# Kernel tuning notes

Measured on AMD Instinct MI355X. Metric: run time of the kernel, lower is better.

The kernel has to match this reference:

```python
import jax, jax.numpy as jnp
import numpy as np

N, E, B = 16384, 65536, 32
D_IN, ED, H, L = 4, 5, 64, 3  # node feat, edge feat, hidden=output, num layers
NEG_SLOPE = 0.1
EPS = 1e-5


def _leaky(v):
    return jnp.where(v > 0, v, NEG_SLOPE * v)


def setup_inputs() -> dict:
    key = jax.random.key(0)
    ks = jax.random.split(key, 32)
    s = 0.05
    inp = {
        'x': jax.random.normal(ks[0], (N, D_IN), jnp.float32),
        'edge_index': jax.random.randint(ks[1], (2, E), 0, N),
        'edge_attr': jax.random.normal(ks[2], (E, ED), jnp.float32),
        'batch': jnp.sort(jax.random.randint(ks[3], (N,), 0, B)),
        # input projection Linear(4 -> H)
        'W_in': s * jax.random.normal(ks[4], (H, D_IN), jnp.float32),
        'b_in': jnp.zeros((H,), jnp.float32),
        # per-layer edge MLP: Linear(ED->H), Linear(H->H), Linear(H->H*H); stacked over L
        'ew1': s * jax.random.normal(ks[5], (L, H, ED), jnp.float32),
        'eb1': jnp.zeros((L, H), jnp.float32),
        'ew2': s * jax.random.normal(ks[6], (L, H, H), jnp.float32),
        'eb2': jnp.zeros((L, H), jnp.float32),
        'ew3': s * jax.random.normal(ks[7], (L, H * H, H), jnp.float32),
        'eb3': jnp.zeros((L, H * H), jnp.float32),
        # NNConv root weight + bias per layer
        'root_w': s * jax.random.normal(ks[8], (L, H, H), jnp.float32),
        'root_b': jnp.zeros((L, H), jnp.float32),
        # LayerNorm per layer
        'ln_g': jnp.ones((L, H), jnp.float32),
        'ln_b': jnp.zeros((L, H), jnp.float32),
        # prediction head: Linear(H->H), Linear(H->H//2), Linear(H//2->1)
        'pw1': s * jax.random.normal(ks[9], (H, H), jnp.float32),
        'pb1': jnp.zeros((H,), jnp.float32),
        'pw2': s * jax.random.normal(ks[10], (H // 2, H), jnp.float32),
        'pb2': jnp.zeros((H // 2,), jnp.float32),
        'pw3': s * jax.random.normal(ks[11], (1, H // 2), jnp.float32),
        'pb3': jnp.zeros((1,), jnp.float32),
    }
    return inp


def reference(x, edge_index, edge_attr, batch, W_in, b_in, ew1, eb1, ew2, eb2,
              ew3, eb3, root_w, root_b, ln_g, ln_b, pw1, pb1, pw2, pb2, pw3, pb3):
    src, dst = edge_index[0], edge_index[1]
    n_nodes = x.shape[0]
    n_edges = edge_attr.shape[0]
    # in-degree for scatter-mean (PyG yields 0 for isolated nodes)
    deg = jax.ops.segment_sum(jnp.ones((n_edges,), x.dtype), dst, num_segments=n_nodes)
    deg = jnp.maximum(deg, 1.0)[:, None]

    # input projection (dropout = identity in eval)
    h = _leaky(x @ W_in.T + b_in)

    for l in range(L):
        # edge MLP -> per-edge weight matrix [E, H, H]
        e = _leaky(edge_attr @ ew1[l].T + eb1[l])
        e = _leaky(e @ ew2[l].T + eb2[l])
        Wf = (e @ ew3[l].T + eb3[l]).reshape(n_edges, H, H)
        # message = x_src @ W_edge, scatter-mean to dst
        msg = jnp.einsum('ei,eio->eo', h[src], Wf)
        agg = jax.ops.segment_sum(msg, dst, num_segments=n_nodes) / deg
        out = agg + h @ root_w[l].T + root_b[l]
        # LayerNorm (post-norm)
        mu = out.mean(-1, keepdims=True)
        var = ((out - mu) ** 2).mean(-1, keepdims=True)
        out = (out - mu) * jax.lax.rsqrt(var + EPS) * ln_g[l] + ln_b[l]
        # activation + (identity) dropout + residual (in==out for all layers)
        h = _leaky(out) + h

    # global mean pool over graphs
    pooled = jax.ops.segment_sum(h, batch, num_segments=B)
    cnt = jax.ops.segment_sum(jnp.ones((n_nodes,), h.dtype), batch, num_segments=B)
    pooled = pooled / jnp.maximum(cnt, 1.0)[:, None]

    # prediction head
    p = _leaky(pooled @ pw1.T + pb1)
    p = _leaky(p @ pw2.T + pb2)
    pred = (p @ pw3.T + pb3).squeeze(-1)  # [B]
    return pred
```

## Files before the change

kernel.cpp:

```cpp
#include <hip/hip_runtime.h>
#include <hip/hip_bf16.h>

#define N_NODES 16384
#define N_EDGES 65536
#define NB      32
#define H       64
#define NLAYERS 3
#define NEG     0.1f
#define LN_EPS  1e-5f

typedef _Float16 f16;
typedef _Float16 f16x2 __attribute__((ext_vector_type(2)));
typedef _Float16 f16x8 __attribute__((ext_vector_type(8)));
typedef __fp16   hf16x2 __attribute__((ext_vector_type(2)));
typedef float    f32x16 __attribute__((ext_vector_type(16)));

union F16x8 { f16x8 v; f16x2 p[4]; int4 i4; int2 i2[2]; };
union F16x2U { f16x2 h2; hf16x2 raw; unsigned int u; };
union F16U   { f16 h; unsigned short u; };

__device__ __forceinline__ f16x2 pkrtz(float a, float b) {
    F16x2U t; t.raw = __builtin_amdgcn_cvt_pkrtz(a, b); return t.h2;
}
__device__ __forceinline__ float leaky(float v) { return v > 0.f ? v : NEG * v; }

__global__ __launch_bounds__(256) void k_setup(const float* __restrict__ x,
                                               const float* __restrict__ Win,
                                               const float* __restrict__ bin,
                                               const int* __restrict__ dst,
                                               const float* __restrict__ ew3,
                                               const float* __restrict__ eb3,
                                               float* __restrict__ h,
                                               float* __restrict__ deg,
                                               f16* __restrict__ Bp) {
    int bid = blockIdx.x;
    if (bid < 4096) {
        int t = bid * 256 + threadIdx.x;
        int n = t >> 6, j = t & 63;
        const float* xr = x + n * 4;
        const float* wr = Win + j * 4;
        float v = bin[j] + xr[0] * wr[0] + xr[1] * wr[1] + xr[2] * wr[2] + xr[3] * wr[3];
        h[t] = leaky(v);
    } else if (bid < 4352) {
        int e = (bid - 4096) * 256 + threadIdx.x;
        atomicAdd(&deg[dst[e]], 1.0f);
    } else {
        int tg    = (bid - 4352) * 256 + threadIdx.x;
        int lane  = tg & 63;
        int gslot = tg >> 6;
        int l     = gslot / 520;
        int slot  = gslot - l * 520;
        const float* ew3l = ew3 + (size_t)l * 262144;
        const float* eb3l = eb3 + (size_t)l * 4096;
        int i   = slot >> 3;
        int rem = slot & 7;
        int ks  = rem >> 1;
        int oq  = rem & 1;
        int o   = oq * 32 + (lane & 31);
        int k0  = ks * 16 + (lane >> 5) * 8;
        float v[8];
        if (i < 64) {
            const float* s = ew3l + ((size_t)(i * 64 + o)) * 64 + k0;
            float4 a = ((const float4*)s)[0];
            float4 b = ((const float4*)s)[1];
            v[0] = a.x; v[1] = a.y; v[2] = a.z; v[3] = a.w;
            v[4] = b.x; v[5] = b.y; v[6] = b.z; v[7] = b.w;
        } else {
#pragma unroll
            for (int j = 0; j < 8; j++) v[j] = eb3l[(k0 + j) * 64 + o];
        }
        union { int4 i4; f16 a[8]; } out;
#pragma unroll
        for (int j = 0; j < 8; j++) out.a[j] = (f16)v[j];
        *(int4*)(Bp + (size_t)l * 266240 + (size_t)slot * 512 + lane * 8) = out.i4;
    }
}

#define HS_STRIDE 76

__device__ __forceinline__ void loadB8(const f16* __restrict__ Bp, int c, int oq, int lane, F16x8* dstB) {
    const f16* base = Bp + (((size_t)(c * 16 + oq)) << 9) + lane * 8;
#pragma unroll
    for (int di = 0; di < 2; di++)
#pragma unroll
        for (int ks = 0; ks < 4; ks++)
            dstB[di * 4 + ks].i4 = *(const int4*)(base + ((di * 8 + ks * 2) << 9));
}
__device__ __forceinline__ void loadB4(const f16* __restrict__ Bp, int oq, int lane, F16x8* dstB) {
    const f16* base = Bp + (((size_t)(512 + oq)) << 9) + lane * 8;
#pragma unroll
    for (int ks = 0; ks < 4; ks++)
        dstB[ks].i4 = *(const int4*)(base + ((ks * 2) << 9));
}

__device__ __forceinline__ void msg_chunk2(int c, const F16x8* __restrict__ B,
                                           const unsigned short* hp0,
                                           const unsigned short* hp1,
                                           const f16x2 (*e2p)[4][4], f32x16* CC) {
    unsigned int rr0 = *(const unsigned int*)(hp0 + 2 * c);
    unsigned int rr1 = *(const unsigned int*)(hp1 + 2 * c);
    F16x2U h00, h01, h10, h11;
    h00.u = __builtin_amdgcn_perm(rr0, rr0, 0x01000100u);
    h10.u = __builtin_amdgcn_perm(rr0, rr0, 0x03020302u);
    h01.u = __builtin_amdgcn_perm(rr1, rr1, 0x01000100u);
    h11.u = __builtin_amdgcn_perm(rr1, rr1, 0x03020302u);
#pragma unroll
    for (int ks = 0; ks < 4; ks++) {
        F16x8 A00, A01, A10, A11;
#pragma unroll
        for (int r = 0; r < 4; r++) {
            A00.p[r] = h00.h2 * e2p[0][ks][r];
            A01.p[r] = h01.h2 * e2p[1][ks][r];
            A10.p[r] = h10.h2 * e2p[0][ks][r];
            A11.p[r] = h11.h2 * e2p[1][ks][r];
        }
        CC[0] = __builtin_amdgcn_mfma_f32_32x32x16_f16(A00.v, B[0 * 4 + ks].v, CC[0], 0, 0, 0);
        CC[1] = __builtin_amdgcn_mfma_f32_32x32x16_f16(A01.v, B[0 * 4 + ks].v, CC[1], 0, 0, 0);
        CC[2] = __builtin_amdgcn_mfma_f32_32x32x16_f16(A10.v, B[1 * 4 + ks].v, CC[2], 0, 0, 0);
        CC[3] = __builtin_amdgcn_mfma_f32_32x32x16_f16(A11.v, B[1 * 4 + ks].v, CC[3], 0, 0, 0);
    }
}

__global__ __launch_bounds__(256, 2) void k_msg(const float* __restrict__ h,
                                                const float* __restrict__ ea,
                                                const float* __restrict__ w1,
                                                const float* __restrict__ b1,
                                                const float* __restrict__ w2,
                                                const float* __restrict__ b2,
                                                const f16* __restrict__ Bp,
                                                const int* __restrict__ src,
                                                const int* __restrict__ dst,
                                                float* __restrict__ agg) {
    __shared__ __align__(16) unsigned short hsL[128 * HS_STRIDE];
    __shared__ __align__(16) unsigned short e1L[128 * 72];
    __shared__ __align__(16) unsigned short e2L[128 * 72];
    __shared__ float eas[128 * 8];
    __shared__ int dstL[128];

    const int t    = threadIdx.x;
    const int lane = t & 63;
    const int w    = t >> 6;
    const int eh   = w >> 1, oq = w & 1;
    const int m    = lane & 31;
    const int kp   = lane >> 5;
    const int eb   = blockIdx.x * 128;

    for (int idx = t; idx < 640; idx += 256) {
        int r = idx / 5, d = idx - r * 5;
        eas[r * 8 + d] = ea[(size_t)eb * 5 + idx];
    }
    {
        int e    = t >> 1;
        int half = t & 1;
        int nsrc = src[eb + e];
        const float4* hr = (const float4*)(h + (size_t)nsrc * 64 + half * 32);
        unsigned int* hrow = (unsigned int*)hsL + e * (HS_STRIDE / 2) + half * 16;
#pragma unroll
        for (int q = 0; q < 8; q++) {
            float4 v = hr[q];
            F16x2U p0, p1;
            p0.raw = __builtin_amdgcn_cvt_pkrtz(v.x, v.y);
            p1.raw = __builtin_amdgcn_cvt_pkrtz(v.z, v.w);
            hrow[q * 2 + 0] = p0.u;
            hrow[q * 2 + 1] = p1.u;
        }
        if (t < 128) dstL[t] = dst[eb + t];
    }
    __syncthreads();

    {
        int kk = t & 63;
        int eg = t >> 6;
        float w1r[5];
#pragma unroll
        for (int d = 0; d < 5; d++) w1r[d] = w1[kk * 5 + d];
        float b1r = b1[kk];
#pragma unroll 4
        for (int g = 0; g < 32; g++) {
            int row = eg * 32 + g;
            float4 a4 = *(const float4*)(eas + row * 8);
            float a5 = eas[row * 8 + 4];
            float v = b1r + a4.x * w1r[0] + a4.y * w1r[1] + a4.z * w1r[2] + a4.w * w1r[3] + a5 * w1r[4];
            F16U z; z.h = (f16)leaky(v);
            e1L[row * 72 + kk] = z.u;
        }
    }
    __syncthreads();

    {
        F16x8 W2f[4];
#pragma unroll
        for (int ks = 0; ks < 4; ks++) {
            const float* s = w2 + (size_t)(oq * 32 + m) * 64 + ks * 16 + kp * 8;
            float4 a = ((const float4*)s)[0];
            float4 b = ((const float4*)s)[1];
            W2f[ks].p[0] = pkrtz(a.x, a.y);
            W2f[ks].p[1] = pkrtz(a.z, a.w);
            W2f[ks].p[2] = pkrtz(b.x, b.y);
            W2f[ks].p[3] = pkrtz(b.z, b.w);
        }
        float b2r = b2[oq * 32 + m];
#pragma unroll
        for (int tt = 0; tt < 2; tt++) {
            f32x16 C2 = {0,0,0,0,0,0,0,0,0,0,0,0,0,0,0,0};
#pragma unroll
            for (int ks = 0; ks < 4; ks++) {
                F16x8 A;
                A.i4 = *(const int4*)(e1L + (size_t)((eh * 2 + tt) * 32 + m) * 72 + ks * 16 + kp * 8);
                C2 = __builtin_amdgcn_mfma_f32_32x32x16_f16(A.v, W2f[ks].v, C2, 0, 0, 0);
            }
#pragma unroll
            for (int reg = 0; reg < 16; reg++) {
                int r = (reg & 3) + 8 * (reg >> 2) + 4 * kp;
                F16U z; z.h = (f16)leaky(C2[reg] + b2r);
                e2L[((eh * 2 + tt) * 32 + r) * 72 + oq * 32 + m] = z.u;
            }
        }
    }
    __syncthreads();

    f16x2 e2p[2][4][4];
#pragma unroll
    for (int tt = 0; tt < 2; tt++) {
#pragma unroll
        for (int ks = 0; ks < 4; ks++) {
            F16x8 q;
            q.i4 = *(const int4*)(e2L + (size_t)((eh * 2 + tt) * 32 + m) * 72 + ks * 16 + kp * 8);
            e2p[tt][ks][0] = q.p[0]; e2p[tt][ks][1] = q.p[1];
            e2p[tt][ks][2] = q.p[2]; e2p[tt][ks][3] = q.p[3];
        }
    }

    f32x16 CC[4];
#pragma unroll
    for (int q = 0; q < 4; q++)
#pragma unroll
        for (int r = 0; r < 16; r++) CC[q][r] = 0.f;

    const unsigned short* hp0 = hsL + ((eh * 2 + 0) * 32 + m) * HS_STRIDE;
    const unsigned short* hp1 = hsL + ((eh * 2 + 1) * 32 + m) * HS_STRIDE;

    F16x8 B0[8], B1[8];
    loadB8(Bp, 0, oq, lane, B0);
    loadB8(Bp, 1, oq, lane, B1);
    for (int it = 0; it < 15; it++) {
        int c = it * 2;
        msg_chunk2(c,     B0, hp0, hp1, e2p, CC);  loadB8(Bp, c + 2, oq, lane, B0);
        msg_chunk2(c + 1, B1, hp0, hp1, e2p, CC);  loadB8(Bp, c + 3, oq, lane, B1);
    }
    msg_chunk2(30, B0, hp0, hp1, e2p, CC);
    loadB4(Bp, oq, lane, B0);
    msg_chunk2(31, B1, hp0, hp1, e2p, CC);

#pragma unroll
    for (int ks = 0; ks < 4; ks++) {
        int koff = (ks * 16 + kp * 8) * 2;
        const char* r0p = (const char*)hsL + (size_t)((eh * 2 + 0) * 32 + m) * (HS_STRIDE * 2) + koff;
        const char* r1p = (const char*)hsL + (size_t)((eh * 2 + 1) * 32 + m) * (HS_STRIDE * 2) + koff;
        F16x8 A0, A1;
        A0.i2[0] = *(const int2*)(r0p); A0.i2[1] = *(const int2*)(r0p + 8);
        A1.i2[0] = *(const int2*)(r1p); A1.i2[1] = *(const int2*)(r1p + 8);
        CC[0] = __builtin_amdgcn_mfma_f32_32x32x16_f16(A0.v, B0[ks].v, CC[0], 0, 0, 0);
        CC[1] = __builtin_amdgcn_mfma_f32_32x32x16_f16(A1.v, B0[ks].v, CC[1], 0, 0, 0);
    }

    int o = oq * 32 + m;
#pragma unroll
    for (int reg = 0; reg < 16; reg++) {
        int r = (reg & 3) + 8 * (reg >> 2) + 4 * kp;
        atomicAdd(&agg[(size_t)dstL[(eh * 2 + 0) * 32 + r] * 64 + o], CC[0][reg] + CC[2][reg]);
    }
#pragma unroll
    for (int reg = 0; reg < 16; reg++) {
        int r = (reg & 3) + 8 * (reg >> 2) + 4 * kp;
        atomicAdd(&agg[(size_t)dstL[(eh * 2 + 1) * 32 + r] * 64 + o], CC[1][reg] + CC[3][reg]);
    }
}

__global__ __launch_bounds__(256) void k_node(const float* __restrict__ agg,
                                              const float* __restrict__ deg,
                                              const float* __restrict__ rw,
                                              const float* __restrict__ rb,
                                              const float* __restrict__ lg,
                                              const float* __restrict__ lb,
                                              float* __restrict__ h,
                                              const int* __restrict__ batch,
                                              float* __restrict__ pooled,
                                              int last) {
    __shared__ __align__(16) unsigned short hA[64 * 72];
    __shared__ float outL[64][68];
    int t = threadIdx.x;
    int nb = blockIdx.x * 64;
    int lane = t & 63, w = t >> 6;
    int nq = w >> 1, oq = w & 1;
    int m = lane & 31, kp = lane >> 5;

    {
        int r = t >> 2, c0 = (t & 3) * 16;
        const float4* hr = (const float4*)(h + (size_t)(nb + r) * 64 + c0);
        unsigned int* drow = (unsigned int*)hA + r * 36 + c0 / 2;
#pragma unroll
        for (int q = 0; q < 4; q++) {
            float4 v = hr[q];
            F16x2U p0, p1;
            p0.raw = __builtin_amdgcn_cvt_pkrtz(v.x, v.y);
            p1.raw = __builtin_amdgcn_cvt_pkrtz(v.z, v.w);
            drow[q * 2] = p0.u; drow[q * 2 + 1] = p1.u;
        }
    }
    F16x8 Bf[4];
#pragma unroll
    for (int ks = 0; ks < 4; ks++) {
        const float* s = rw + (size_t)(oq * 32 + m) * 64 + ks * 16 + kp * 8;
        float4 a = ((const float4*)s)[0];
        float4 b = ((const float4*)s)[1];
        Bf[ks].p[0] = pkrtz(a.x, a.y);
        Bf[ks].p[1] = pkrtz(a.z, a.w);
        Bf[ks].p[2] = pkrtz(b.x, b.y);
        Bf[ks].p[3] = pkrtz(b.z, b.w);
    }
    __syncthreads();

    f32x16 C = {0,0,0,0,0,0,0,0,0,0,0,0,0,0,0,0};
#pragma unroll
    for (int ks = 0; ks < 4; ks++) {
        F16x8 A;
        A.i4 = *(const int4*)(hA + (size_t)(nq * 32 + m) * 72 + ks * 16 + kp * 8);
        C = __builtin_amdgcn_mfma_f32_32x32x16_f16(A.v, Bf[ks].v, C, 0, 0, 0);
    }

    int o = oq * 32 + m;
#pragma unroll
    for (int reg = 0; reg < 16; reg++) {
        int r = (reg & 3) + 8 * (reg >> 2) + 4 * kp;
        int n = nq * 32 + r;
        outL[n][o] = C[reg] + rb[o] + agg[(size_t)(nb + n) * 64 + o] / fmaxf(deg[nb + n], 1.0f);
    }
    __syncthreads();

    float gj = lg[lane], bj = lb[lane];
    float accp = 0.f;
    int cur = batch[nb + w * 16];
    for (int q = 0; q < 16; q++) {
        int n = w * 16 + q;
        float v = outL[n][lane];
        float mu = v;
#pragma unroll
        for (int msk = 32; msk > 0; msk >>= 1) mu += __shfl_xor(mu, msk);
        mu *= (1.f / 64.f);
        float d = v - mu;
        float var = d * d;
#pragma unroll
        for (int msk = 32; msk > 0; msk >>= 1) var += __shfl_xor(var, msk);
        var *= (1.f / 64.f);
        float ov = d * rsqrtf(var + LN_EPS) * gj + bj;
        float hn = leaky(ov) + h[(size_t)(nb + n) * 64 + lane];
        h[(size_t)(nb + n) * 64 + lane] = hn;
        if (last) {
            int b = batch[nb + n];
            if (b != cur) { atomicAdd(&pooled[cur * 64 + lane], accp); accp = 0.f; cur = b; }
            accp += hn;
        }
    }
    if (last) atomicAdd(&pooled[cur * 64 + lane], accp);
}

__global__ __launch_bounds__(256) void k_head(const float* __restrict__ pooled,
                                              const int* __restrict__ batch,
                                              const float* __restrict__ pw1, const float* __restrict__ pb1,
                                              const float* __restrict__ pw2, const float* __restrict__ pb2,
                                              const float* __restrict__ pw3, const float* __restrict__ pb3,
                                              float* __restrict__ out) {
    __shared__ float cntL[32];
    __shared__ float ps[32][64];
    __shared__ float p1[32][64];
    __shared__ float p2[32][32];
    int t = threadIdx.x;
    if (t < 32) cntL[t] = 0.f;
    __syncthreads();
    {
        const int4* bp4 = (const int4*)(batch + t * 64);
        int cur = batch[t * 64];
        float c = 0.f;
        for (int q = 0; q < 16; q++) {
            int4 b4 = bp4[q];
            int bs[4] = { b4.x, b4.y, b4.z, b4.w };
#pragma unroll
            for (int e = 0; e < 4; e++) {
                if (bs[e] != cur) { atomicAdd(&cntL[cur], c); cur = bs[e]; c = 0.f; }
                c += 1.f;
            }
        }
        atomicAdd(&cntL[cur], c);
    }
    __syncthreads();
    for (int idx = t; idx < 2048; idx += 256) {
        int b = idx >> 6, j = idx & 63;
        ps[b][j] = pooled[idx] / fmaxf(cntL[b], 1.0f);
    }
    __syncthreads();
    for (int idx = t; idx < 2048; idx += 256) {
        int b = idx >> 6, j = idx & 63;
        float v = pb1[j];
#pragma unroll 8
        for (int i = 0; i < 64; i++) v += ps[b][i] * pw1[j * 64 + i];
        p1[b][j] = leaky(v);
    }
    __syncthreads();
    for (int idx = t; idx < 1024; idx += 256) {
        int b = idx >> 5, j = idx & 31;
        float v = pb2[j];
#pragma unroll 8
        for (int i = 0; i < 64; i++) v += p1[b][i] * pw2[j * 64 + i];
        p2[b][j] = leaky(v);
    }
    __syncthreads();
    if (t < 32) {
        float v = pb3[0];
#pragma unroll 8
        for (int i = 0; i < 32; i++) v += p2[t][i] * pw3[i];
        out[t] = v;
    }
}

extern "C" void kernel_launch(void* const* d_in, const int* in_sizes, int n_in,
                              void* d_out, int out_size, void* d_ws, size_t ws_size,
                              hipStream_t stream) {
    const float* x    = (const float*)d_in[0];
    const int*   eidx = (const int*)  d_in[1];
    const float* ea   = (const float*)d_in[2];
    const int*   bat  = (const int*)  d_in[3];
    const float* Win  = (const float*)d_in[4];
    const float* bin  = (const float*)d_in[5];
    const float* ew1  = (const float*)d_in[6];
    const float* eb1  = (const float*)d_in[7];
    const float* ew2  = (const float*)d_in[8];
    const float* eb2  = (const float*)d_in[9];
    const float* ew3  = (const float*)d_in[10];
    const float* eb3  = (const float*)d_in[11];
    const float* rw   = (const float*)d_in[12];
    const float* rb   = (const float*)d_in[13];
    const float* lg   = (const float*)d_in[14];
    const float* lb   = (const float*)d_in[15];
    const float* pw1  = (const float*)d_in[16];
    const float* pb1  = (const float*)d_in[17];
    const float* pw2  = (const float*)d_in[18];
    const float* pb2  = (const float*)d_in[19];
    const float* pw3  = (const float*)d_in[20];
    const float* pb3  = (const float*)d_in[21];
    float* out = (float*)d_out;

    float* ws     = (float*)d_ws;
    float* h      = ws;
    float* agg    = ws + 1048576;
    float* deg    = ws + 4194304;
    float* pooled = ws + 4210688;
    f16*   Bp     = (f16*)(ws + 4212800);

    const int* srcp = eidx;
    const int* dstp = eidx + N_EDGES;

    (void)hipMemsetAsync(agg, 0, (size_t)3164224 * sizeof(float), stream);

    k_setup<<<4742, 256, 0, stream>>>(x, Win, bin, dstp, ew3, eb3, h, deg, Bp);

    for (int l = 0; l < NLAYERS; l++) {
        float* agg_l = agg + (size_t)l * N_NODES * H;
        k_msg <<<N_EDGES / 128, 256, 0, stream>>>(h, ea, ew1 + l * 320, eb1 + l * 64,
                                                  ew2 + l * 4096, eb2 + l * 64,
                                                  Bp + (size_t)l * 266240,
                                                  srcp, dstp, agg_l);
        k_node<<<N_NODES / 64, 256, 0, stream>>>(agg_l, deg, rw + l * 4096, rb + l * 64,
                                                 lg + l * 64, lb + l * 64, h,
                                                 bat, pooled, l == NLAYERS - 1 ? 1 : 0);
    }

    k_head<<<1, 256, 0, stream>>>(pooled, bat, pw1, pb1, pw2, pb2, pw3, pb3, out);
}
```

Measured before the change: 323.1 us.

## Fuse all layers into one persistent cooperative kernel with grid syncs

Measured after the change: 596.5 us. 84.6% more time.

```diff
diff --git a/kernel.cpp b/kernel.cpp
--- a/kernel.cpp
+++ b/kernel.cpp
@@ -1,5 +1,8 @@
 #include <hip/hip_runtime.h>
 #include <hip/hip_bf16.h>
+#include <hip/hip_cooperative_groups.h>
+
+namespace cg = cooperative_groups;
 
 #define N_NODES 16384
 #define N_EDGES 65536
@@ -24,59 +27,26 @@
 }
 __device__ __forceinline__ float leaky(float v) { return v > 0.f ? v : NEG * v; }
 
-__global__ __launch_bounds__(256) void k_setup(const float* __restrict__ x,
-                                               const float* __restrict__ Win,
-                                               const float* __restrict__ bin,
-                                               const int* __restrict__ dst,
-                                               const float* __restrict__ ew3,
-                                               const float* __restrict__ eb3,
-                                               float* __restrict__ h,
-                                               float* __restrict__ deg,
-                                               f16* __restrict__ Bp) {
-    int bid = blockIdx.x;
-    if (bid < 4096) {
-        int t = bid * 256 + threadIdx.x;
-        int n = t >> 6, j = t & 63;
-        const float* xr = x + n * 4;
-        const float* wr = Win + j * 4;
-        float v = bin[j] + xr[0] * wr[0] + xr[1] * wr[1] + xr[2] * wr[2] + xr[3] * wr[3];
-        h[t] = leaky(v);
-    } else if (bid < 4352) {
-        int e = (bid - 4096) * 256 + threadIdx.x;
-        atomicAdd(&deg[dst[e]], 1.0f);
-    } else {
-        int tg    = (bid - 4352) * 256 + threadIdx.x;
-        int lane  = tg & 63;
-        int gslot = tg >> 6;
-        int l     = gslot / 520;
-        int slot  = gslot - l * 520;
-        const float* ew3l = ew3 + (size_t)l * 262144;
-        const float* eb3l = eb3 + (size_t)l * 4096;
-        int i   = slot >> 3;
-        int rem = slot & 7;
-        int ks  = rem >> 1;
-        int oq  = rem & 1;
-        int o   = oq * 32 + (lane & 31);
-        int k0  = ks * 16 + (lane >> 5) * 8;
-        float v[8];
-        if (i < 64) {
-            const float* s = ew3l + ((size_t)(i * 64 + o)) * 64 + k0;
-            float4 a = ((const float4*)s)[0];
-            float4 b = ((const float4*)s)[1];
-            v[0] = a.x; v[1] = a.y; v[2] = a.z; v[3] = a.w;
-            v[4] = b.x; v[5] = b.y; v[6] = b.z; v[7] = b.w;
-        } else {
-#pragma unroll
-            for (int j = 0; j < 8; j++) v[j] = eb3l[(k0 + j) * 64 + o];
-        }
-        union { int4 i4; f16 a[8]; } out;
-#pragma unroll
-        for (int j = 0; j < 8; j++) out.a[j] = (f16)v[j];
-        *(int4*)(Bp + (size_t)l * 266240 + (size_t)slot * 512 + lane * 8) = out.i4;
-    }
-}
-
 #define HS_STRIDE 76
+
+struct MsgSh {
+    unsigned short hsL[128 * HS_STRIDE];
+    unsigned short e1L[128 * 72];
+    unsigned short e2L[128 * 72];
+    float eas[128 * 8];
+    int dstL[128];
+};
+struct NodeSh {
+    unsigned short hA[64 * 72];
+    float outL[64][68];
+};
+struct HeadSh {
+    float cntL[32];
+    float ps[32][64];
+    float p1[32][64];
+    float p2[32][32];
+};
+union ShU { MsgSh m[2]; NodeSh n; HeadSh hd; };
 
 __device__ __forceinline__ void loadB8(const f16* __restrict__ Bp, int c, int oq, int lane, F16x8* dstB) {
     const f16* base = Bp + (((size_t)(c * 16 + oq)) << 9) + lane * 8;
@@ -121,40 +91,33 @@
     }
 }
 
-__global__ __launch_bounds__(256, 2) void k_msg(const float* __restrict__ h,
-                                                const float* __restrict__ ea,
-                                                const float* __restrict__ w1,
-                                                const float* __restrict__ b1,
-                                                const float* __restrict__ w2,
-                                                const float* __restrict__ b2,
-                                                const f16* __restrict__ Bp,
-                                                const int* __restrict__ src,
-                                                const int* __restrict__ dst,
-                                                float* __restrict__ agg) {
-    __shared__ __align__(16) unsigned short hsL[128 * HS_STRIDE];
-    __shared__ __align__(16) unsigned short e1L[128 * 72];
-    __shared__ __align__(16) unsigned short e2L[128 * 72];
-    __shared__ float eas[128 * 8];
-    __shared__ int dstL[128];
-
-    const int t    = threadIdx.x;
-    const int lane = t & 63;
-    const int w    = t >> 6;
-    const int eh   = w >> 1, oq = w & 1;
+__device__ void msg_phase(MsgSh& S, int th, int ebh,
+                          const float* __restrict__ h,
+                          const float* __restrict__ ea,
+                          const float* __restrict__ w1,
+                          const float* __restrict__ b1,
+                          const float* __restrict__ w2,
+                          const float* __restrict__ b2,
+                          const f16* __restrict__ Bp,
+                          const int* __restrict__ src,
+                          const int* __restrict__ dst,
+                          float* __restrict__ agg) {
+    const int lane = th & 63;
+    const int wl   = th >> 6;
+    const int eh   = wl >> 1, oq = wl & 1;
     const int m    = lane & 31;
     const int kp   = lane >> 5;
-    const int eb   = blockIdx.x * 128;
-
-    for (int idx = t; idx < 640; idx += 256) {
+
+    for (int idx = th; idx < 640; idx += 256) {
         int r = idx / 5, d = idx - r * 5;
-        eas[r * 8 + d] = ea[(size_t)eb * 5 + idx];
+        S.eas[r * 8 + d] = ea[(size_t)ebh * 5 + idx];
     }
     {
-        int e    = t >> 1;
-        int half = t & 1;
-        int nsrc = src[eb + e];
-        const float4* hr = (const float4*)(h + (size_t)nsrc * 64 + half * 32);
-        unsigned int* hrow = (unsigned int*)hsL + e * (HS_STRIDE / 2) + half * 16;
+        int e    = th >> 1;
+        int half2 = th & 1;
+        int nsrc = src[ebh + e];
+        const float4* hr = (const float4*)(h + (size_t)nsrc * 64 + half2 * 32);
+        unsigned int* hrow = (unsigned int*)S.hsL + e * (HS_STRIDE / 2) + half2 * 16;
 #pragma unroll
         for (int q = 0; q < 8; q++) {
             float4 v = hr[q];
@@ -164,13 +127,13 @@
             hrow[q * 2 + 0] = p0.u;
             hrow[q * 2 + 1] = p1.u;
         }
-        if (t < 128) dstL[t] = dst[eb + t];
+        if (th < 128) S.dstL[th] = dst[ebh + th];
     }
     __syncthreads();
 
     {
-        int kk = t & 63;
-        int eg = t >> 6;
+        int kk = th & 63;
+        int eg = th >> 6;
         float w1r[5];
 #pragma unroll
         for (int d = 0; d < 5; d++) w1r[d] = w1[kk * 5 + d];
@@ -178,11 +141,11 @@
 #pragma unroll 4
         for (int g = 0; g < 32; g++) {
             int row = eg * 32 + g;
-            float4 a4 = *(const float4*)(eas + row * 8);
-            float a5 = eas[row * 8 + 4];
+            float4 a4 = *(const float4*)(S.eas + row * 8);
+            float a5 = S.eas[row * 8 + 4];
             float v = b1r + a4.x * w1r[0] + a4.y * w1r[1] + a4.z * w1r[2] + a4.w * w1r[3] + a5 * w1r[4];
             F16U z; z.h = (f16)leaky(v);
-            e1L[row * 72 + kk] = z.u;
+            S.e1L[row * 72 + kk] = z.u;
         }
     }
     __syncthreads();
@@ -206,14 +169,14 @@
 #pragma unroll
             for (int ks = 0; ks < 4; ks++) {
                 F16x8 A;
-                A.i4 = *(const int4*)(e1L + (size_t)((eh * 2 + tt) * 32 + m) * 72 + ks * 16 + kp * 8);
+                A.i4 = *(const int4*)(S.e1L + (size_t)((eh * 2 + tt) * 32 + m) * 72 + ks * 16 + kp * 8);
                 C2 = __builtin_amdgcn_mfma_f32_32x32x16_f16(A.v, W2f[ks].v, C2, 0, 0, 0);
             }
 #pragma unroll
             for (int reg = 0; reg < 16; reg++) {
                 int r = (reg & 3) + 8 * (reg >> 2) + 4 * kp;
                 F16U z; z.h = (f16)leaky(C2[reg] + b2r);
-                e2L[((eh * 2 + tt) * 32 + r) * 72 + oq * 32 + m] = z.u;
+                S.e2L[((eh * 2 + tt) * 32 + r) * 72 + oq * 32 + m] = z.u;
             }
         }
     }
@@ -225,7 +188,7 @@
 #pragma unroll
         for (int ks = 0; ks < 4; ks++) {
             F16x8 q;
-            q.i4 = *(const int4*)(e2L + (size_t)((eh * 2 + tt) * 32 + m) * 72 + ks * 16 + kp * 8);
+            q.i4 = *(const int4*)(S.e2L + (size_t)((eh * 2 + tt) * 32 + m) * 72 + ks * 16 + kp * 8);
             e2p[tt][ks][0] = q.p[0]; e2p[tt][ks][1] = q.p[1];
             e2p[tt][ks][2] = q.p[2]; e2p[tt][ks][3] = q.p[3];
         }
@@ -237,8 +200,8 @@
 #pragma unroll
         for (int r = 0; r < 16; r++) CC[q][r] = 0.f;
 
-    const unsigned short* hp0 = hsL + ((eh * 2 + 0) * 32 + m) * HS_STRIDE;
-    const unsigned short* hp1 = hsL + ((eh * 2 + 1) * 32 + m) * HS_STRIDE;
+    const unsigned short* hp0 = S.hsL + ((eh * 2 + 0) * 32 + m) * HS_STRIDE;
+    const unsigned short* hp1 = S.hsL + ((eh * 2 + 1) * 32 + m) * HS_STRIDE;
 
     F16x8 B0[8], B1[8];
     loadB8(Bp, 0, oq, lane, B0);
@@ -255,8 +218,8 @@
 #pragma unroll
     for (int ks = 0; ks < 4; ks++) {
         int koff = (ks * 16 + kp * 8) * 2;
-        const char* r0p = (const char*)hsL + (size_t)((eh * 2 + 0) * 32 + m) * (HS_STRIDE * 2) + koff;
-        const char* r1p = (const char*)hsL + (size_t)((eh * 2 + 1) * 32 + m) * (HS_STRIDE * 2) + koff;
+        const char* r0p = (const char*)S.hsL + (size_t)((eh * 2 + 0) * 32 + m) * (HS_STRIDE * 2) + koff;
+        const char* r1p = (const char*)S.hsL + (size_t)((eh * 2 + 1) * 32 + m) * (HS_STRIDE * 2) + koff;
         F16x8 A0, A1;
         A0.i2[0] = *(const int2*)(r0p); A0.i2[1] = *(const int2*)(r0p + 8);
         A1.i2[0] = *(const int2*)(r1p); A1.i2[1] = *(const int2*)(r1p + 8);
@@ -268,158 +231,223 @@
 #pragma unroll
     for (int reg = 0; reg < 16; reg++) {
         int r = (reg & 3) + 8 * (reg >> 2) + 4 * kp;
-        atomicAdd(&agg[(size_t)dstL[(eh * 2 + 0) * 32 + r] * 64 + o], CC[0][reg] + CC[2][reg]);
+        atomicAdd(&agg[(size_t)S.dstL[(eh * 2 + 0) * 32 + r] * 64 + o], CC[0][reg] + CC[2][reg]);
     }
 #pragma unroll
     for (int reg = 0; reg < 16; reg++) {
         int r = (reg & 3) + 8 * (reg >> 2) + 4 * kp;
-        atomicAdd(&agg[(size_t)dstL[(eh * 2 + 1) * 32 + r] * 64 + o], CC[1][reg] + CC[3][reg]);
-    }
-}
-
-__global__ __launch_bounds__(256) void k_node(const float* __restrict__ agg,
-                                              const float* __restrict__ deg,
-                                              const float* __restrict__ rw,
-                                              const float* __restrict__ rb,
-                                              const float* __restrict__ lg,
-                                              const float* __restrict__ lb,
-                                              float* __restrict__ h,
-                                              const int* __restrict__ batch,
-                                              float* __restrict__ pooled,
-                                              int last) {
-    __shared__ __align__(16) unsigned short hA[64 * 72];
-    __shared__ float outL[64][68];
-    int t = threadIdx.x;
-    int nb = blockIdx.x * 64;
-    int lane = t & 63, w = t >> 6;
-    int nq = w >> 1, oq = w & 1;
-    int m = lane & 31, kp = lane >> 5;
+        atomicAdd(&agg[(size_t)S.dstL[(eh * 2 + 1) * 32 + r] * 64 + o], CC[1][reg] + CC[3][reg]);
+    }
+}
+
+__global__ __launch_bounds__(512, 2) void k_fused(
+    const float* __restrict__ x, const float* __restrict__ ea,
+    const int* __restrict__ src, const int* __restrict__ dst, const int* __restrict__ bat,
+    const float* __restrict__ Win, const float* __restrict__ bin,
+    const float* __restrict__ ew1, const float* __restrict__ eb1,
+    const float* __restrict__ ew2, const float* __restrict__ eb2,
+    const float* __restrict__ ew3, const float* __restrict__ eb3,
+    const float* __restrict__ rw, const float* __restrict__ rb,
+    const float* __restrict__ lg, const float* __restrict__ lb,
+    const float* __restrict__ pw1, const float* __restrict__ pb1,
+    const float* __restrict__ pw2, const float* __restrict__ pb2,
+    const float* __restrict__ pw3, const float* __restrict__ pb3,
+    float* __restrict__ h, float* __restrict__ agg, float* __restrict__ deg,
+    float* __restrict__ pooled, f16* __restrict__ Bp, float* __restrict__ out) {
+
+    __shared__ __align__(16) ShU sh;
+    cg::grid_group grid = cg::this_grid();
+
+    const int t    = threadIdx.x;
+    const int lane = t & 63;
+    const int w    = t >> 6;
+    const int half = t >> 8;
+    const int th   = t & 255;
 
     {
-        int r = t >> 2, c0 = (t & 3) * 16;
-        const float4* hr = (const float4*)(h + (size_t)(nb + r) * 64 + c0);
-        unsigned int* drow = (unsigned int*)hA + r * 36 + c0 / 2;
-#pragma unroll
-        for (int q = 0; q < 4; q++) {
-            float4 v = hr[q];
-            F16x2U p0, p1;
-            p0.raw = __builtin_amdgcn_cvt_pkrtz(v.x, v.y);
-            p1.raw = __builtin_amdgcn_cvt_pkrtz(v.z, v.w);
-            drow[q * 2] = p0.u; drow[q * 2 + 1] = p1.u;
-        }
-    }
-    F16x8 Bf[4];
-#pragma unroll
-    for (int ks = 0; ks < 4; ks++) {
-        const float* s = rw + (size_t)(oq * 32 + m) * 64 + ks * 16 + kp * 8;
-        float4 a = ((const float4*)s)[0];
-        float4 b = ((const float4*)s)[1];
-        Bf[ks].p[0] = pkrtz(a.x, a.y);
-        Bf[ks].p[1] = pkrtz(a.z, a.w);
-        Bf[ks].p[2] = pkrtz(b.x, b.y);
-        Bf[ks].p[3] = pkrtz(b.z, b.w);
-    }
-    __syncthreads();
-
-    f32x16 C = {0,0,0,0,0,0,0,0,0,0,0,0,0,0,0,0};
-#pragma unroll
-    for (int ks = 0; ks < 4; ks++) {
-        F16x8 A;
-        A.i4 = *(const int4*)(hA + (size_t)(nq * 32 + m) * 72 + ks * 16 + kp * 8);
-        C = __builtin_amdgcn_mfma_f32_32x32x16_f16(A.v, Bf[ks].v, C, 0, 0, 0);
-    }
-
-    int o = oq * 32 + m;
-#pragma unroll
-    for (int reg = 0; reg < 16; reg++) {
-        int r = (reg & 3) + 8 * (reg >> 2) + 4 * kp;
-        int n = nq * 32 + r;
-        outL[n][o] = C[reg] + rb[o] + agg[(size_t)(nb + n) * 64 + o] / fmaxf(deg[nb + n], 1.0f);
-    }
-    __syncthreads();
-
-    float gj = lg[lane], bj = lb[lane];
-    float accp = 0.f;
-    int cur = batch[nb + w * 16];
-    for (int q = 0; q < 16; q++) {
-        int n = w * 16 + q;
-        float v = outL[n][lane];
-        float mu = v;
-#pragma unroll
-        for (int msk = 32; msk > 0; msk >>= 1) mu += __shfl_xor(mu, msk);
-        mu *= (1.f / 64.f);
-        float d = v - mu;
-        float var = d * d;
-#pragma unroll
-        for (int msk = 32; msk > 0; msk >>= 1) var += __shfl_xor(var, msk);
-        var *= (1.f / 64.f);
-        float ov = d * rsqrtf(var + LN_EPS) * gj + bj;
-        float hn = leaky(ov) + h[(size_t)(nb + n) * 64 + lane];
-        h[(size_t)(nb + n) * 64 + lane] = hn;
-        if (last) {
-            int b = batch[nb + n];
-            if (b != cur) { atomicAdd(&pooled[cur * 64 + lane], accp); accp = 0.f; cur = b; }
-            accp += hn;
-        }
-    }
-    if (last) atomicAdd(&pooled[cur * 64 + lane], accp);
-}
-
-__global__ __launch_bounds__(256) void k_head(const float* __restrict__ pooled,
-                                              const int* __restrict__ batch,
-                                              const float* __restrict__ pw1, const float* __restrict__ pb1,
-                                              const float* __restrict__ pw2, const float* __restrict__ pb2,
-                                              const float* __restrict__ pw3, const float* __restrict__ pb3,
-                                              float* __restrict__ out) {
-    __shared__ float cntL[32];
-    __shared__ float ps[32][64];
-    __shared__ float p1[32][64];
-    __shared__ float p2[32][32];
-    int t = threadIdx.x;
-    if (t < 32) cntL[t] = 0.f;
-    __syncthreads();
-    {
-        const int4* bp4 = (const int4*)(batch + t * 64);
-        int cur = batch[t * 64];
-        float c = 0.f;
-        for (int q = 0; q < 16; q++) {
-            int4 b4 = bp4[q];
-            int bs[4] = { b4.x, b4.y, b4.z, b4.w };
-#pragma unroll
-            for (int e = 0; e < 4; e++) {
-                if (bs[e] != cur) { atomicAdd(&cntL[cur], c); cur = bs[e]; c = 0.f; }
-                c += 1.f;
-            }
-        }
-        atomicAdd(&cntL[cur], c);
-    }
-    __syncthreads();
-    for (int idx = t; idx < 2048; idx += 256) {
-        int b = idx >> 6, j = idx & 63;
-        ps[b][j] = pooled[idx] / fmaxf(cntL[b], 1.0f);
-    }
-    __syncthreads();
-    for (int idx = t; idx < 2048; idx += 256) {
-        int b = idx >> 6, j = idx & 63;
-        float v = pb1[j];
+        int tg = blockIdx.x * 512 + t;
+#pragma unroll
+        for (int r = 0; r < 8; r++) {
+            int idx = r * 131072 + tg;
+            int n = idx >> 6, j = idx & 63;
+            const float* xr = x + n * 4;
+            const float* wr = Win + j * 4;
+            float v = bin[j] + xr[0] * wr[0] + xr[1] * wr[1] + xr[2] * wr[2] + xr[3] * wr[3];
+            h[idx] = leaky(v);
+        }
+        if (tg < N_EDGES) atomicAdd(&deg[dst[tg]], 1.0f);
+        int wid = blockIdx.x * 8 + w;
+        if (wid < 1560) {
+            int l    = wid / 520;
+            int slot = wid - l * 520;
+            const float* ew3l = ew3 + (size_t)l * 262144;
+            const float* eb3l = eb3 + (size_t)l * 4096;
+            int i   = slot >> 3;
+            int rem = slot & 7;
+            int ks  = rem >> 1;
+            int oq  = rem & 1;
+            int o   = oq * 32 + (lane & 31);
+            int k0  = ks * 16 + (lane >> 5) * 8;
+            float v[8];
+            if (i < 64) {
+                const float* s = ew3l + ((size_t)(i * 64 + o)) * 64 + k0;
+                float4 a = ((const float4*)s)[0];
+                float4 b = ((const float4*)s)[1];
+                v[0] = a.x; v[1] = a.y; v[2] = a.z; v[3] = a.w;
+                v[4] = b.x; v[5] = b.y; v[6] = b.z; v[7] = b.w;
+            } else {
+#pragma unroll
+                for (int j = 0; j < 8; j++) v[j] = eb3l[(k0 + j) * 64 + o];
+            }
+            union { int4 i4; f16 a[8]; } ov;
+#pragma unroll
+            for (int j = 0; j < 8; j++) ov.a[j] = (f16)v[j];
+            *(int4*)(Bp + (size_t)l * 266240 + (size_t)slot * 512 + lane * 8) = ov.i4;
+        }
+    }
+    grid.sync();
+
+    for (int l = 0; l < NLAYERS; l++) {
+        float* agg_l = agg + (size_t)l * N_NODES * H;
+        msg_phase(sh.m[half], th, blockIdx.x * 256 + half * 128,
+                  h, ea, ew1 + l * 320, eb1 + l * 64,
+                  ew2 + l * 4096, eb2 + l * 64,
+                  Bp + (size_t)l * 266240, src, dst, agg_l);
+        grid.sync();
+
+        {
+            NodeSh& N = sh.n;
+            const float* rwl = rw + l * 4096;
+            const float* rbl = rb + l * 64;
+            const float* lgl = lg + l * 64;
+            const float* lbl = lb + l * 64;
+            int last = (l == NLAYERS - 1) ? 1 : 0;
+            int nb = blockIdx.x * 64;
+            int wl = th >> 6;
+            int nq = wl >> 1, oq = wl & 1;
+            int m = lane & 31, kp = lane >> 5;
+
+            F16x8 Bf[4];
+            if (half == 0) {
+                int r = th >> 2, c0 = (th & 3) * 16;
+                const float4* hr = (const float4*)(h + (size_t)(nb + r) * 64 + c0);
+                unsigned int* drow = (unsigned int*)N.hA + r * 36 + c0 / 2;
+#pragma unroll
+                for (int q = 0; q < 4; q++) {
+                    float4 v = hr[q];
+                    F16x2U p0, p1;
+                    p0.raw = __builtin_amdgcn_cvt_pkrtz(v.x, v.y);
+                    p1.raw = __builtin_amdgcn_cvt_pkrtz(v.z, v.w);
+                    drow[q * 2] = p0.u; drow[q * 2 + 1] = p1.u;
+                }
+#pragma unroll
+                for (int ks = 0; ks < 4; ks++) {
+                    const float* s = rwl + (size_t)(oq * 32 + m) * 64 + ks * 16 + kp * 8;
+                    float4 a = ((const float4*)s)[0];
+                    float4 b = ((const float4*)s)[1];
+                    Bf[ks].p[0] = pkrtz(a.x, a.y);
+                    Bf[ks].p[1] = pkrtz(a.z, a.w);
+                    Bf[ks].p[2] = pkrtz(b.x, b.y);
+                    Bf[ks].p[3] = pkrtz(b.z, b.w);
+                }
+            }
+            __syncthreads();
+            if (half == 0) {
+                f32x16 C = {0,0,0,0,0,0,0,0,0,0,0,0,0,0,0,0};
+#pragma unroll
+                for (int ks = 0; ks < 4; ks++) {
+                    F16x8 A;
+                    A.i4 = *(const int4*)(N.hA + (size_t)(nq * 32 + m) * 72 + ks * 16 + kp * 8);
+                    C = __builtin_amdgcn_mfma_f32_32x32x16_f16(A.v, Bf[ks].v, C, 0, 0, 0);
+                }
+                int o = oq * 32 + m;
+#pragma unroll
+                for (int reg = 0; reg < 16; reg++) {
+                    int r = (reg & 3) + 8 * (reg >> 2) + 4 * kp;
+                    int n = nq * 32 + r;
+                    N.outL[n][o] = C[reg] + rbl[o] + agg_l[(size_t)(nb + n) * 64 + o] / fmaxf(deg[nb + n], 1.0f);
+                }
+            }
+            __syncthreads();
+            if (half == 0) {
+                float gj = lgl[lane], bj = lbl[lane];
+                float accp = 0.f;
+                int cur = bat[nb + wl * 16];
+                for (int q = 0; q < 16; q++) {
+                    int n = wl * 16 + q;
+                    float v = N.outL[n][lane];
+                    float mu = v;
+#pragma unroll
+                    for (int msk = 32; msk > 0; msk >>= 1) mu += __shfl_xor(mu, msk);
+                    mu *= (1.f / 64.f);
+                    float d = v - mu;
+                    float var = d * d;
+#pragma unroll
+                    for (int msk = 32; msk > 0; msk >>= 1) var += __shfl_xor(var, msk);
+                    var *= (1.f / 64.f);
+                    float ov = d * rsqrtf(var + LN_EPS) * gj + bj;
+                    float hn = leaky(ov) + h[(size_t)(nb + n) * 64 + lane];
+                    h[(size_t)(nb + n) * 64 + lane] = hn;
+                    if (last) {
+                        int b = bat[nb + n];
+                        if (b != cur) { atomicAdd(&pooled[cur * 64 + lane], accp); accp = 0.f; cur = b; }
+                        accp += hn;
+                    }
+                }
+                if (last) atomicAdd(&pooled[cur * 64 + lane], accp);
+            }
+            __syncthreads();
+        }
+        grid.sync();
+    }
+
+    if (blockIdx.x == 0) {
+        HeadSh& Hh = sh.hd;
+        if (t < 32) Hh.cntL[t] = 0.f;
+        __syncthreads();
+        {
+            const int4* bp4 = (const int4*)(bat + t * 32);
+            int cur = bat[t * 32];
+            float c = 0.f;
+            for (int q = 0; q < 8; q++) {
+                int4 b4 = bp4[q];
+                int bs[4] = { b4.x, b4.y, b4.z, b4.w };
+#pragma unroll
+                for (int e = 0; e < 4; e++) {
+                    if (bs[e] != cur) { atomicAdd(&Hh.cntL[cur], c); cur = bs[e]; c = 0.f; }
+                    c += 1.f;
+                }
+            }
+            atomicAdd(&Hh.cntL[cur], c);
+        }
+        __syncthreads();
+        for (int idx = t; idx < 2048; idx += 512) {
+            int b = idx >> 6, j = idx & 63;
+            Hh.ps[b][j] = pooled[idx] / fmaxf(Hh.cntL[b], 1.0f);
+        }
+        __syncthreads();
+        for (int idx = t; idx < 2048; idx += 512) {
+            int b = idx >> 6, j = idx & 63;
+            float v = pb1[j];
 #pragma unroll 8
-        for (int i = 0; i < 64; i++) v += ps[b][i] * pw1[j * 64 + i];
-        p1[b][j] = leaky(v);
-    }
-    __syncthreads();
-    for (int idx = t; idx < 1024; idx += 256) {
-        int b = idx >> 5, j = idx & 31;
-        float v = pb2[j];
+            for (int i = 0; i < 64; i++) v += Hh.ps[b][i] * pw1[j * 64 + i];
+            Hh.p1[b][j] = leaky(v);
+        }
+        __syncthreads();
+        for (int idx = t; idx < 1024; idx += 512) {
+            int b = idx >> 5, j = idx & 31;
+            float v = pb2[j];
 #pragma unroll 8
-        for (int i = 0; i < 64; i++) v += p1[b][i] * pw2[j * 64 + i];
-        p2[b][j] = leaky(v);
-    }
-    __syncthreads();
-    if (t < 32) {
-        float v = pb3[0];
+            for (int i = 0; i < 64; i++) v += Hh.p1[b][i] * pw2[j * 64 + i];
+            Hh.p2[b][j] = leaky(v);
+        }
+        __syncthreads();
+        if (t < 32) {
+            float v = pb3[0];
 #pragma unroll 8
-        for (int i = 0; i < 32; i++) v += p2[t][i] * pw3[i];
-        out[t] = v;
+            for (int i = 0; i < 32; i++) v += Hh.p2[t][i] * pw3[i];
+            out[t] = v;
+        }
     }
 }
 
@@ -462,18 +490,16 @@
 
     (void)hipMemsetAsync(agg, 0, (size_t)3164224 * sizeof(float), stream);
 
-    k_setup<<<4742, 256, 0, stream>>>(x, Win, bin, dstp, ew3, eb3, h, deg, Bp);
-
-    for (int l = 0; l < NLAYERS; l++) {
-        float* agg_l = agg + (size_t)l * N_NODES * H;
-        k_msg <<<N_EDGES / 128, 256, 0, stream>>>(h, ea, ew1 + l * 320, eb1 + l * 64,
-                                                  ew2 + l * 4096, eb2 + l * 64,
-                                                  Bp + (size_t)l * 266240,
-                                                  srcp, dstp, agg_l);
-        k_node<<<N_NODES / 64, 256, 0, stream>>>(agg_l, deg, rw + l * 4096, rb + l * 64,
-                                                 lg + l * 64, lb + l * 64, h,
-                                                 bat, pooled, l == NLAYERS - 1 ? 1 : 0);
-    }
-
-    k_head<<<1, 256, 0, stream>>>(pooled, bat, pw1, pb1, pw2, pb2, pw3, pb3, out);
-}
+    void* args[] = {
+        (void*)&x, (void*)&ea, (void*)&srcp, (void*)&dstp, (void*)&bat,
+        (void*)&Win, (void*)&bin,
+        (void*)&ew1, (void*)&eb1, (void*)&ew2, (void*)&eb2,
+        (void*)&ew3, (void*)&eb3,
+        (void*)&rw, (void*)&rb, (void*)&lg, (void*)&lb,
+        (void*)&pw1, (void*)&pb1, (void*)&pw2, (void*)&pb2,
+        (void*)&pw3, (void*)&pb3,
+        (void*)&h, (void*)&agg, (void*)&deg, (void*)&pooled, (void*)&Bp, (void*)&out
+    };
+    (void)hipLaunchCooperativeKernel((void*)k_fused, dim3(256), dim3(512),
+                                     args, 0, stream);
+}
```

## Fuse input projection into layer-0 kernels and head into last node kernel

Applied to the files above, without the earlier changes.

Measured after the change: 356.2 us. 1.1x slower.

```diff
diff --git a/kernel.cpp b/kernel.cpp
--- a/kernel.cpp
+++ b/kernel.cpp
@@ -24,28 +24,17 @@
 }
 __device__ __forceinline__ float leaky(float v) { return v > 0.f ? v : NEG * v; }
 
-__global__ __launch_bounds__(256) void k_setup(const float* __restrict__ x,
-                                               const float* __restrict__ Win,
-                                               const float* __restrict__ bin,
-                                               const int* __restrict__ dst,
+__global__ __launch_bounds__(256) void k_setup(const int* __restrict__ dst,
                                                const float* __restrict__ ew3,
                                                const float* __restrict__ eb3,
-                                               float* __restrict__ h,
                                                float* __restrict__ deg,
                                                f16* __restrict__ Bp) {
     int bid = blockIdx.x;
-    if (bid < 4096) {
-        int t = bid * 256 + threadIdx.x;
-        int n = t >> 6, j = t & 63;
-        const float* xr = x + n * 4;
-        const float* wr = Win + j * 4;
-        float v = bin[j] + xr[0] * wr[0] + xr[1] * wr[1] + xr[2] * wr[2] + xr[3] * wr[3];
-        h[t] = leaky(v);
-    } else if (bid < 4352) {
-        int e = (bid - 4096) * 256 + threadIdx.x;
+    if (bid < 256) {
+        int e = bid * 256 + threadIdx.x;
         atomicAdd(&deg[dst[e]], 1.0f);
     } else {
-        int tg    = (bid - 4352) * 256 + threadIdx.x;
+        int tg    = (bid - 256) * 256 + threadIdx.x;
         int lane  = tg & 63;
         int gslot = tg >> 6;
         int l     = gslot / 520;
@@ -122,6 +111,10 @@
 }
 
 __global__ __launch_bounds__(256, 2) void k_msg(const float* __restrict__ h,
+                                                const float* __restrict__ x,
+                                                const float* __restrict__ Win,
+                                                const float* __restrict__ bin,
+                                                int first,
                                                 const float* __restrict__ ea,
                                                 const float* __restrict__ w1,
                                                 const float* __restrict__ b1,
@@ -153,16 +146,30 @@
         int e    = t >> 1;
         int half = t & 1;
         int nsrc = src[eb + e];
-        const float4* hr = (const float4*)(h + (size_t)nsrc * 64 + half * 32);
         unsigned int* hrow = (unsigned int*)hsL + e * (HS_STRIDE / 2) + half * 16;
-#pragma unroll
-        for (int q = 0; q < 8; q++) {
-            float4 v = hr[q];
-            F16x2U p0, p1;
-            p0.raw = __builtin_amdgcn_cvt_pkrtz(v.x, v.y);
-            p1.raw = __builtin_amdgcn_cvt_pkrtz(v.z, v.w);
-            hrow[q * 2 + 0] = p0.u;
-            hrow[q * 2 + 1] = p1.u;
+        if (first) {
+            float4 xr = *(const float4*)(x + (size_t)nsrc * 4);
+            const float4* wr = (const float4*)Win + half * 32;
+            const float* bb = bin + half * 32;
+#pragma unroll
+            for (int q = 0; q < 16; q++) {
+                float4 w0 = wr[q * 2], w1 = wr[q * 2 + 1];
+                float v0 = bb[q * 2]     + xr.x * w0.x + xr.y * w0.y + xr.z * w0.z + xr.w * w0.w;
+                float v1 = bb[q * 2 + 1] + xr.x * w1.x + xr.y * w1.y + xr.z * w1.z + xr.w * w1.w;
+                F16x2U p; p.raw = __builtin_amdgcn_cvt_pkrtz(leaky(v0), leaky(v1));
+                hrow[q] = p.u;
+            }
+        } else {
+            const float4* hr = (const float4*)(h + (size_t)nsrc * 64 + half * 32);
+#pragma unroll
+            for (int q = 0; q < 8; q++) {
+                float4 v = hr[q];
+                F16x2U p0, p1;
+                p0.raw = __builtin_amdgcn_cvt_pkrtz(v.x, v.y);
+                p1.raw = __builtin_amdgcn_cvt_pkrtz(v.z, v.w);
+                hrow[q * 2 + 0] = p0.u;
+                hrow[q * 2 + 1] = p1.u;
+            }
         }
         if (t < 128) dstL[t] = dst[eb + t];
     }
@@ -277,6 +284,10 @@
     }
 }
 
+struct NodeSh { unsigned short hA[64 * 72]; float outL[64][68]; };
+struct HeadSh { float cntL[32]; float ps[32][64]; float p1[32][64]; float p2[32][32]; };
+union NodeU { NodeSh n; HeadSh hd; };
+
 __global__ __launch_bounds__(256) void k_node(const float* __restrict__ agg,
                                               const float* __restrict__ deg,
                                               const float* __restrict__ rw,
@@ -284,11 +295,19 @@
                                               const float* __restrict__ lg,
                                               const float* __restrict__ lb,
                                               float* __restrict__ h,
+                                              const float* __restrict__ x,
+                                              const float* __restrict__ Win,
+                                              const float* __restrict__ bin,
                                               const int* __restrict__ batch,
                                               float* __restrict__ pooled,
-                                              int last) {
-    __shared__ __align__(16) unsigned short hA[64 * 72];
-    __shared__ float outL[64][68];
+                                              int first, int last,
+                                              int* __restrict__ done,
+                                              const float* __restrict__ pw1, const float* __restrict__ pb1,
+                                              const float* __restrict__ pw2, const float* __restrict__ pb2,
+                                              const float* __restrict__ pw3, const float* __restrict__ pb3,
+                                              float* __restrict__ out) {
+    __shared__ __align__(16) NodeU sh;
+    __shared__ int isLastBlk;
     int t = threadIdx.x;
     int nb = blockIdx.x * 64;
     int lane = t & 63, w = t >> 6;
@@ -297,15 +316,29 @@
 
     {
         int r = t >> 2, c0 = (t & 3) * 16;
-        const float4* hr = (const float4*)(h + (size_t)(nb + r) * 64 + c0);
-        unsigned int* drow = (unsigned int*)hA + r * 36 + c0 / 2;
-#pragma unroll
-        for (int q = 0; q < 4; q++) {
-            float4 v = hr[q];
-            F16x2U p0, p1;
-            p0.raw = __builtin_amdgcn_cvt_pkrtz(v.x, v.y);
-            p1.raw = __builtin_amdgcn_cvt_pkrtz(v.z, v.w);
-            drow[q * 2] = p0.u; drow[q * 2 + 1] = p1.u;
+        unsigned int* drow = (unsigned int*)sh.n.hA + r * 36 + c0 / 2;
+        if (first) {
+            float4 xr = *(const float4*)(x + (size_t)(nb + r) * 4);
+            const float4* wrp = (const float4*)Win + c0;
+            const float* bb = bin + c0;
+#pragma unroll
+            for (int q = 0; q < 8; q++) {
+                float4 w0 = wrp[q * 2], w1 = wrp[q * 2 + 1];
+                float v0 = bb[q * 2]     + xr.x * w0.x + xr.y * w0.y + xr.z * w0.z + xr.w * w0.w;
+                float v1 = bb[q * 2 + 1] + xr.x * w1.x + xr.y * w1.y + xr.z * w1.z + xr.w * w1.w;
+                F16x2U p; p.raw = __builtin_amdgcn_cvt_pkrtz(leaky(v0), leaky(v1));
+                drow[q] = p.u;
+            }
+        } else {
+            const float4* hr = (const float4*)(h + (size_t)(nb + r) * 64 + c0);
+#pragma unroll
+            for (int q = 0; q < 4; q++) {
+                float4 v = hr[q];
+                F16x2U p0, p1;
+                p0.raw = __builtin_amdgcn_cvt_pkrtz(v.x, v.y);
+                p1.raw = __builtin_amdgcn_cvt_pkrtz(v.z, v.w);
+                drow[q * 2] = p0.u; drow[q * 2 + 1] = p1.u;
+            }
         }
     }
     F16x8 Bf[4];
@@ -325,7 +358,7 @@
 #pragma unroll
     for (int ks = 0; ks < 4; ks++) {
         F16x8 A;
-        A.i4 = *(const int4*)(hA + (size_t)(nq * 32 + m) * 72 + ks * 16 + kp * 8);
+        A.i4 = *(const int4*)(sh.n.hA + (size_t)(nq * 32 + m) * 72 + ks * 16 + kp * 8);
         C = __builtin_amdgcn_mfma_f32_32x32x16_f16(A.v, Bf[ks].v, C, 0, 0, 0);
     }
 
@@ -334,92 +367,104 @@
     for (int reg = 0; reg < 16; reg++) {
         int r = (reg & 3) + 8 * (reg >> 2) + 4 * kp;
         int n = nq * 32 + r;
-        outL[n][o] = C[reg] + rb[o] + agg[(size_t)(nb + n) * 64 + o] / fmaxf(deg[nb + n], 1.0f);
+        sh.n.outL[n][o] = C[reg] + rb[o] + agg[(size_t)(nb + n) * 64 + o] / fmaxf(deg[nb + n], 1.0f);
     }
     __syncthreads();
 
-    float gj = lg[lane], bj = lb[lane];
-    float accp = 0.f;
-    int cur = batch[nb + w * 16];
-    for (int q = 0; q < 16; q++) {
-        int n = w * 16 + q;
-        float v = outL[n][lane];
-        float mu = v;
-#pragma unroll
-        for (int msk = 32; msk > 0; msk >>= 1) mu += __shfl_xor(mu, msk);
-        mu *= (1.f / 64.f);
-        float d = v - mu;
-        float var = d * d;
-#pragma unroll
-        for (int msk = 32; msk > 0; msk >>= 1) var += __shfl_xor(var, msk);
-        var *= (1.f / 64.f);
-        float ov = d * rsqrtf(var + LN_EPS) * gj + bj;
-        float hn = leaky(ov) + h[(size_t)(nb + n) * 64 + lane];
-        h[(size_t)(nb + n) * 64 + lane] = hn;
-        if (last) {
-            int b = batch[nb + n];
-            if (b != cur) { atomicAdd(&pooled[cur * 64 + lane], accp); accp = 0.f; cur = b; }
-            accp += hn;
-        }
-    }
-    if (last) atomicAdd(&pooled[cur * 64 + lane], accp);
-}
-
-__global__ __launch_bounds__(256) void k_head(const float* __restrict__ pooled,
-                                              const int* __restrict__ batch,
-                                              const float* __restrict__ pw1, const float* __restrict__ pb1,
-                                              const float* __restrict__ pw2, const float* __restrict__ pb2,
-                                              const float* __restrict__ pw3, const float* __restrict__ pb3,
-                                              float* __restrict__ out) {
-    __shared__ float cntL[32];
-    __shared__ float ps[32][64];
-    __shared__ float p1[32][64];
-    __shared__ float p2[32][32];
-    int t = threadIdx.x;
-    if (t < 32) cntL[t] = 0.f;
-    __syncthreads();
     {
-        const int4* bp4 = (const int4*)(batch + t * 64);
-        int cur = batch[t * 64];
-        float c = 0.f;
+        float gj = lg[lane], bj = lb[lane];
+        float wr0 = 0.f, wr1 = 0.f, wr2 = 0.f, wr3 = 0.f, br = 0.f;
+        if (first) {
+            wr0 = Win[lane * 4 + 0]; wr1 = Win[lane * 4 + 1];
+            wr2 = Win[lane * 4 + 2]; wr3 = Win[lane * 4 + 3];
+            br  = bin[lane];
+        }
+        float accp = 0.f;
+        int cur = batch[nb + w * 16];
         for (int q = 0; q < 16; q++) {
-            int4 b4 = bp4[q];
-            int bs[4] = { b4.x, b4.y, b4.z, b4.w };
-#pragma unroll
-            for (int e = 0; e < 4; e++) {
-                if (bs[e] != cur) { atomicAdd(&cntL[cur], c); cur = bs[e]; c = 0.f; }
-                c += 1.f;
-            }
-        }
-        atomicAdd(&cntL[cur], c);
-    }
-    __syncthreads();
-    for (int idx = t; idx < 2048; idx += 256) {
-        int b = idx >> 6, j = idx & 63;
-        ps[b][j] = pooled[idx] / fmaxf(cntL[b], 1.0f);
-    }
-    __syncthreads();
-    for (int idx = t; idx < 2048; idx += 256) {
-        int b = idx >> 6, j = idx & 63;
-        float v = pb1[j];
+            int n = w * 16 + q;
+            float v = sh.n.outL[n][lane];
+            float mu = v;
+#pragma unroll
+            for (int msk = 32; msk > 0; msk >>= 1) mu += __shfl_xor(mu, msk);
+            mu *= (1.f / 64.f);
+            float d = v - mu;
+            float var = d * d;
+#pragma unroll
+            for (int msk = 32; msk > 0; msk >>= 1) var += __shfl_xor(var, msk);
+            var *= (1.f / 64.f);
+            float ov = d * rsqrtf(var + LN_EPS) * gj + bj;
+            float hprev;
+            if (first) {
+                float4 xr = *(const float4*)(x + (size_t)(nb + n) * 4);
+                hprev = leaky(br + xr.x * wr0 + xr.y * wr1 + xr.z * wr2 + xr.w * wr3);
+            } else {
+                hprev = h[(size_t)(nb + n) * 64 + lane];
+            }
+            float hn = leaky(ov) + hprev;
+            h[(size_t)(nb + n) * 64 + lane] = hn;
+            if (last) {
+                int b = batch[nb + n];
+                if (b != cur) { atomicAdd(&pooled[cur * 64 + lane], accp); accp = 0.f; cur = b; }
+                accp += hn;
+            }
+        }
+        if (last) atomicAdd(&pooled[cur * 64 + lane], accp);
+    }
+
+    if (last) {
+        __threadfence();
+        if (t == 0) isLastBlk = (atomicAdd(done, 1) == (int)gridDim.x - 1) ? 1 : 0;
+        __syncthreads();
+        if (!isLastBlk) return;
+
+        HeadSh& Hh = sh.hd;
+        if (t < 32) Hh.cntL[t] = 0.f;
+        __syncthreads();
+        {
+            const int4* bp4 = (const int4*)(batch + t * 64);
+            int cur = batch[t * 64];
+            float c = 0.f;
+            for (int q = 0; q < 16; q++) {
+                int4 b4 = bp4[q];
+                int bs[4] = { b4.x, b4.y, b4.z, b4.w };
+#pragma unroll
+                for (int e = 0; e < 4; e++) {
+                    if (bs[e] != cur) { atomicAdd(&Hh.cntL[cur], c); cur = bs[e]; c = 0.f; }
+                    c += 1.f;
+                }
+            }
+            atomicAdd(&Hh.cntL[cur], c);
+        }
+        __syncthreads();
+        for (int idx = t; idx < 2048; idx += 256) {
+            int b = idx >> 6, j = idx & 63;
+            float pv = atomicAdd(&pooled[idx], 0.0f);
+            Hh.ps[b][j] = pv / fmaxf(Hh.cntL[b], 1.0f);
+        }
+        __syncthreads();
+        for (int idx = t; idx < 2048; idx += 256) {
+            int b = idx >> 6, j = idx & 63;
+            float v = pb1[j];
 #pragma unroll 8
-        for (int i = 0; i < 64; i++) v += ps[b][i] * pw1[j * 64 + i];
-        p1[b][j] = leaky(v);
-    }
-    __syncthreads();
-    for (int idx = t; idx < 1024; idx += 256) {
-        int b = idx >> 5, j = idx & 31;
-        float v = pb2[j];
+            for (int i = 0; i < 64; i++) v += Hh.ps[b][i] * pw1[j * 64 + i];
+            Hh.p1[b][j] = leaky(v);
+        }
+        __syncthreads();
+        for (int idx = t; idx < 1024; idx += 256) {
+            int b = idx >> 5, j = idx & 31;
+            float v = pb2[j];
 #pragma unroll 8
-        for (int i = 0; i < 64; i++) v += p1[b][i] * pw2[j * 64 + i];
-        p2[b][j] = leaky(v);
-    }
-    __syncthreads();
-    if (t < 32) {
-        float v = pb3[0];
+            for (int i = 0; i < 64; i++) v += Hh.p1[b][i] * pw2[j * 64 + i];
+            Hh.p2[b][j] = leaky(v);
+        }
+        __syncthreads();
+        if (t < 32) {
+            float v = pb3[0];
 #pragma unroll 8
-        for (int i = 0; i < 32; i++) v += p2[t][i] * pw3[i];
-        out[t] = v;
+            for (int i = 0; i < 32; i++) v += Hh.p2[t][i] * pw3[i];
+            out[t] = v;
+        }
     }
 }
 
@@ -455,6 +500,7 @@
     float* agg    = ws + 1048576;
     float* deg    = ws + 4194304;
     float* pooled = ws + 4210688;
+    int*   done   = (int*)(ws + 4212736);
     f16*   Bp     = (f16*)(ws + 4212800);
 
     const int* srcp = eidx;
@@ -462,18 +508,21 @@
 
     (void)hipMemsetAsync(agg, 0, (size_t)3164224 * sizeof(float), stream);
 
-    k_setup<<<4742, 256, 0, stream>>>(x, Win, bin, dstp, ew3, eb3, h, deg, Bp);
+    k_setup<<<646, 256, 0, stream>>>(dstp, ew3, eb3, deg, Bp);
 
     for (int l = 0; l < NLAYERS; l++) {
         float* agg_l = agg + (size_t)l * N_NODES * H;
-        k_msg <<<N_EDGES / 128, 256, 0, stream>>>(h, ea, ew1 + l * 320, eb1 + l * 64,
+        int first = (l == 0) ? 1 : 0;
+        int last  = (l == NLAYERS - 1) ? 1 : 0;
+        k_msg <<<N_EDGES / 128, 256, 0, stream>>>(h, x, Win, bin, first,
+                                                  ea, ew1 + l * 320, eb1 + l * 64,
                                                   ew2 + l * 4096, eb2 + l * 64,
                                                   Bp + (size_t)l * 266240,
                                                   srcp, dstp, agg_l);
         k_node<<<N_NODES / 64, 256, 0, stream>>>(agg_l, deg, rw + l * 4096, rb + l * 64,
                                                  lg + l * 64, lb + l * 64, h,
-                                                 bat, pooled, l == NLAYERS - 1 ? 1 : 0);
-    }
-
-    k_head<<<1, 256, 0, stream>>>(pooled, bat, pw1, pb1, pw2, pb2, pw3, pb3, out);
-}
+                                                 x, Win, bin, bat, pooled,
+                                                 first, last, done,
+                                                 pw1, pb1, pw2, pb2, pw3, pb3, out);
+    }
+}
```
